# Performance work log

Measured on AMD Instinct MI355X. Metric: run time of the kernel, lower is better.

Reference implementation:

```python
import jax, jax.numpy as jnp
import numpy as np

B, N, D, H = 8, 512, 512, 8
DK = D // H          # 64
DIM_G = 64           # trigonometric geometry embedding dim
WAVE_LEN = 1000.0


def box_relational_embedding(f_g):
    # f_g: [B, N, 4] -> [B, N, N, 64]
    x_min, y_min, x_max, y_max = [f_g[..., i] for i in range(4)]  # [B,N]
    cx = (x_min + x_max) * 0.5
    cy = (y_min + y_max) * 0.5
    w = x_max - x_min + 1.0
    h = y_max - y_min + 1.0
    # pairwise deltas; divide by w_i / h_i of the row box (broadcast over j)
    dx = jnp.log(jnp.clip(jnp.abs((cx[:, :, None] - cx[:, None, :]) / w[:, :, None]), 0.001))
    dy = jnp.log(jnp.clip(jnp.abs((cy[:, :, None] - cy[:, None, :]) / h[:, :, None]), 0.001))
    dw = jnp.log(w[:, :, None] / w[:, None, :])
    dh = jnp.log(h[:, :, None] / h[:, None, :])
    pos = jnp.stack([dx, dy, dw, dh], axis=-1)  # [B,N,N,4]
    feat_range = jnp.arange(DIM_G // 8, dtype=jnp.float32) / (DIM_G / 8.0)  # [8]
    dim_mat = 1.0 / (WAVE_LEN ** feat_range)  # [8]
    mul = (100.0 * pos)[..., None] * dim_mat  # [B,N,N,4,8]
    mul = mul.reshape(pos.shape[0], pos.shape[1], pos.shape[2], -1)  # [B,N,N,32]
    return jnp.concatenate([jnp.sin(mul), jnp.cos(mul)], axis=-1)  # [B,N,N,64]


def setup_inputs() -> dict:
    key = jax.random.key(0)
    ks = jax.random.split(key, 12)
    s = 1.0 / np.sqrt(D)
    return {
        "input_query": jax.random.normal(ks[0], (B, N, D), jnp.float32),
        "input_key": jax.random.normal(ks[1], (B, N, D), jnp.float32),
        "input_value": jax.random.normal(ks[2], (B, N, D), jnp.float32),
        "input_box": jax.random.uniform(ks[3], (B, N, 4), jnp.float32),
        "mask": jax.random.randint(ks[4], (B, N), 0, 2, jnp.int32),
        "not_objects": jax.random.randint(ks[5], (B, N), 0, 2).astype(jnp.bool_),
        "Wq": jax.random.normal(ks[6], (D, D), jnp.float32) * s,
        "bq": jnp.zeros((D,), jnp.float32),
        "Wk": jax.random.normal(ks[7], (D, D), jnp.float32) * s,
        "bk": jnp.zeros((D,), jnp.float32),
        "Wv": jax.random.normal(ks[8], (D, D), jnp.float32) * s,
        "bv": jnp.zeros((D,), jnp.float32),
        "Wo": jax.random.normal(ks[9], (D, D), jnp.float32) * s,
        "bo": jnp.zeros((D,), jnp.float32),
        "WG": jax.random.normal(ks[10], (H, DIM_G), jnp.float32) * 0.1,
        "bG": jnp.zeros((H,), jnp.float32),
    }


def reference(input_query, input_key, input_value, input_box, mask, not_objects,
              Wq, bq, Wk, bk, Wv, bv, Wo, bo, WG, bG):
    emb = box_relational_embedding(input_box)  # [B,N,N,64]

    def proj(x, W, b):
        return (x @ W + b).reshape(B, N, H, DK).transpose(0, 2, 1, 3)  # [B,H,N,DK]

    q = proj(input_query, Wq, bq)
    k = proj(input_key, Wk, bk)
    v = proj(input_value, Wv, bv)

    scores = jnp.einsum('bhnd,bhmd->bhnm', q, k) / np.sqrt(DK).astype(np.float32)
    scores = jnp.where(mask[:, None, None, :] == 0, -1e9, scores)

    # per-head geometry weights: [B,H,N,N]
    wg = jax.nn.relu(jnp.einsum('bnmg,hg->bhnm', emb, WG) + bG[None, :, None, None])

    # object mask: zero the geometry log-bias where either i or j is not an object
    pair_not_obj = not_objects[:, None, :, None] | not_objects[:, None, None, :]  # [B,1,N,N]
    mask_obj = 1.0 - pair_not_obj.astype(jnp.float32)

    logits = jnp.log(jnp.clip(wg, 1e-6)) * mask_obj + scores
    attn = jax.nn.softmax(logits, axis=-1)  # dropout is identity in eval mode

    out = jnp.einsum('bhnm,bhmd->bhnd', attn, v)
    out = out.transpose(0, 2, 1, 3).reshape(B, N, D)
    return out @ Wo + bo
```

## Files before the change

kernel.cpp:

```cpp
#include <hip/hip_runtime.h>
#include <hip/hip_fp16.h>

#define B_ 8
#define N_ 512
#define D_ 512
#define H_ 8
#define DK_ 64

typedef unsigned int uint;
typedef unsigned short ushort;
typedef __attribute__((ext_vector_type(8))) short short8;
typedef __attribute__((ext_vector_type(8))) _Float16 half8;
typedef __attribute__((ext_vector_type(4))) _Float16 half4;
typedef __attribute__((ext_vector_type(4))) float floatx4;

__device__ __forceinline__ float bf2f(ushort s) { return __uint_as_float(((uint)s) << 16); }
__device__ __forceinline__ ushort f2bf(float f) {
    uint x = __float_as_uint(f);
    return (ushort)((x + 0x7fffu + ((x >> 16) & 1u)) >> 16);
}
__device__ __forceinline__ float blo(uint u) { return __uint_as_float(u << 16); }
__device__ __forceinline__ float bhi(uint u) { return __uint_as_float(u & 0xffff0000u); }
__device__ __forceinline__ float ldf(const void* p, size_t i, int isbf) {
    return isbf ? bf2f(((const ushort*)p)[i]) : ((const float*)p)[i];
}
__device__ __forceinline__ short ldb(const void* p, size_t i, int isbf) {
    return isbf ? (short)(((const ushort*)p)[i]) : (short)f2bf(((const float*)p)[i]);
}
__device__ __forceinline__ float4 ldbox(const void* p, size_t row, int isbf) {
    if (isbf) {
        const uint2 u = ((const uint2*)p)[row];
        return make_float4(blo(u.x), bhi(u.x), blo(u.y), bhi(u.y));
    }
    return ((const float4*)p)[row];
}
__device__ __forceinline__ float flog(float x) {
    return __builtin_amdgcn_logf(x) * 0.69314718056f;
}
__device__ __forceinline__ float fexp(float x) {
    return __builtin_amdgcn_exp2f(x * 1.44269504089f);
}
__device__ __forceinline__ void fsincos_rev(float rev, float* s, float* c) {
    const float fr = rev - floorf(rev);
    *s = __builtin_amdgcn_sinf(fr);
    *c = __builtin_amdgcn_cosf(fr);
}

__global__ __launch_bounds__(256) void probe_dtype(const uint* __restrict__ q,
                                                   int* __restrict__ flag) {
    __shared__ int s[256];
    const int t = threadIdx.x;
    int cnt = 0;
    for (int i = t; i < 4096; i += 256) {
        const uint e = (q[i] >> 7) & 0xffu;
        cnt += (e >= 0x70u && e <= 0x84u) ? 1 : 0;
    }
    s[t] = cnt;
    __syncthreads();
    for (int d = 128; d > 0; d >>= 1) {
        if (t < d) s[t] += s[t + d];
        __syncthreads();
    }
    if (t == 0) *flag = (s[0] > 3276) ? 1 : 0;
}

__global__ __launch_bounds__(256) void transw(const void* __restrict__ w0,
                                              const void* __restrict__ w1,
                                              const void* __restrict__ w2,
                                              const void* __restrict__ w3,
                                              const void* __restrict__ b0,
                                              const void* __restrict__ b1,
                                              const void* __restrict__ b2,
                                              const void* __restrict__ b3,
                                              ushort* __restrict__ wt,
                                              float* __restrict__ biasf,
                                              const int* __restrict__ flagp) {
    const int isbf = *flagp;
    const int z = blockIdx.z;
    const void* W = (z == 0) ? w0 : (z == 1) ? w1 : (z == 2) ? w2 : w3;
    const int n0 = blockIdx.x * 32, k0 = blockIdx.y * 32;
    __shared__ float tile[32][33];
    const int tx = threadIdx.x & 31, ty = threadIdx.x >> 5;
#pragma unroll
    for (int r = 0; r < 4; ++r)
        tile[ty + 8 * r][tx] = ldf(W, (size_t)(k0 + ty + 8 * r) * D_ + n0 + tx, isbf);
    if (blockIdx.x == 0 && blockIdx.y == 0) {
        const void* bz = (z == 0) ? b0 : (z == 1) ? b1 : (z == 2) ? b2 : b3;
        for (int e = threadIdx.x; e < 512; e += 256)
            biasf[z * 512 + e] = ldf(bz, e, isbf);
    }
    __syncthreads();
#pragma unroll
    for (int r = 0; r < 4; ++r)
        wt[(size_t)z * 262144 + (size_t)(n0 + ty + 8 * r) * D_ + k0 + tx] =
            f2bf(tile[tx][ty + 8 * r]);
}

__global__ __launch_bounds__(256) void gemm0(
    const void* __restrict__ A0, const void* __restrict__ A1, const void* __restrict__ A2,
    const ushort* __restrict__ wt, const float* __restrict__ biasf,
    ushort* __restrict__ oq, ushort* __restrict__ ok, ushort* __restrict__ ov,
    const int* __restrict__ flagp) {
    const int isbf = *flagp;
    const int z = blockIdx.z;
    const char* A = (const char*)((z == 0) ? A0 : (z == 1) ? A1 : A2);
    const ushort* W = wt + (size_t)z * 262144;
    const float* bias = biasf + z * 512;
    const int row0 = blockIdx.x * 128, col0 = blockIdx.y * 64;
    const int t = threadIdx.x, wv = t >> 6, lane = t & 63;
    const int m16 = lane & 15, quad = lane >> 4;

    __shared__ ushort As[128][40];
    __shared__ ushort Ws[64][40];
    floatx4 acc[2][4] = {};

    const int ar = t >> 1, ah = t & 1;
    const int wr = t >> 2, wc = (t & 3) * 8;

    float4 pf0, pf1, pf2, pf3;
    short8 ps0, ps1, pw;

    auto loadA = [&](int k0) {
        const size_t e = (size_t)(row0 + ar) * D_ + k0 + ah * 16;
        if (isbf) {
            ps0 = *(const short8*)(A + 2 * e);
            ps1 = *(const short8*)(A + 2 * e + 16);
        } else {
            const float* ap = (const float*)(A + 4 * e);
            pf0 = *(const float4*)(ap);
            pf1 = *(const float4*)(ap + 4);
            pf2 = *(const float4*)(ap + 8);
            pf3 = *(const float4*)(ap + 12);
        }
        pw = *(const short8*)(W + (size_t)(col0 + wr) * D_ + k0 + wc);
    };
    auto stage = [&]() {
        short8 s0, s1;
        if (isbf) {
            s0 = ps0; s1 = ps1;
        } else {
            s0[0] = (short)f2bf(pf0.x); s0[1] = (short)f2bf(pf0.y);
            s0[2] = (short)f2bf(pf0.z); s0[3] = (short)f2bf(pf0.w);
            s0[4] = (short)f2bf(pf1.x); s0[5] = (short)f2bf(pf1.y);
            s0[6] = (short)f2bf(pf1.z); s0[7] = (short)f2bf(pf1.w);
            s1[0] = (short)f2bf(pf2.x); s1[1] = (short)f2bf(pf2.y);
            s1[2] = (short)f2bf(pf2.z); s1[3] = (short)f2bf(pf2.w);
            s1[4] = (short)f2bf(pf3.x); s1[5] = (short)f2bf(pf3.y);
            s1[6] = (short)f2bf(pf3.z); s1[7] = (short)f2bf(pf3.w);
        }
        *(short8*)&As[ar][ah * 16] = s0;
        *(short8*)&As[ar][ah * 16 + 8] = s1;
        *(short8*)&Ws[wr][wc] = pw;
    };

    loadA(0);
    for (int k0 = 0; k0 < D_; k0 += 32) {
        __syncthreads();
        stage();
        __syncthreads();
        if (k0 + 32 < D_) loadA(k0 + 32);

        const short8 a0 = *(const short8*)&As[wv * 32 + m16][quad * 8];
        const short8 a1 = *(const short8*)&As[wv * 32 + 16 + m16][quad * 8];
        const short8 b0 = *(const short8*)&Ws[m16][quad * 8];
        const short8 b1 = *(const short8*)&Ws[16 + m16][quad * 8];
        const short8 b2 = *(const short8*)&Ws[32 + m16][quad * 8];
        const short8 b3 = *(const short8*)&Ws[48 + m16][quad * 8];
        acc[0][0] = __builtin_amdgcn_mfma_f32_16x16x32_bf16(a0, b0, acc[0][0], 0, 0, 0);
        acc[0][1] = __builtin_amdgcn_mfma_f32_16x16x32_bf16(a0, b1, acc[0][1], 0, 0, 0);
        acc[0][2] = __builtin_amdgcn_mfma_f32_16x16x32_bf16(a0, b2, acc[0][2], 0, 0, 0);
        acc[0][3] = __builtin_amdgcn_mfma_f32_16x16x32_bf16(a0, b3, acc[0][3], 0, 0, 0);
        acc[1][0] = __builtin_amdgcn_mfma_f32_16x16x32_bf16(a1, b0, acc[1][0], 0, 0, 0);
        acc[1][1] = __builtin_amdgcn_mfma_f32_16x16x32_bf16(a1, b1, acc[1][1], 0, 0, 0);
        acc[1][2] = __builtin_amdgcn_mfma_f32_16x16x32_bf16(a1, b2, acc[1][2], 0, 0, 0);
        acc[1][3] = __builtin_amdgcn_mfma_f32_16x16x32_bf16(a1, b3, acc[1][3], 0, 0, 0);
    }

#pragma unroll
    for (int mt = 0; mt < 2; ++mt) {
#pragma unroll
        for (int nt = 0; nt < 4; ++nt) {
            const int colg = col0 + nt * 16 + m16;
            const float bi = bias[colg];
            const float v0 = acc[mt][nt][0] + bi, v1 = acc[mt][nt][1] + bi;
            const float v2 = acc[mt][nt][2] + bi, v3 = acc[mt][nt][3] + bi;
            const int rowb = row0 + wv * 32 + mt * 16 + quad * 4;
            if (z == 2) {
                const int bhv = (rowb >> 9) * H_ + (colg >> 6);
                uint2 pk;
                pk.x = (uint)f2bf(v0) | ((uint)f2bf(v1) << 16);
                pk.y = (uint)f2bf(v2) | ((uint)f2bf(v3) << 16);
                *(uint2*)(ov + ((size_t)bhv * DK_ + (colg & 63)) * N_ + (rowb & 511)) = pk;
            } else {
                ushort* o = (z == 0) ? oq : ok;
                const float vv[4] = {v0, v1, v2, v3};
#pragma unroll
                for (int r = 0; r < 4; ++r) {
                    const int row = rowb + r;
                    o[((size_t)((row >> 9) * H_ + (colg >> 6)) * N_ + (row & 511)) * DK_ +
                      (colg & 63)] = f2bf(vv[r]);
                }
            }
        }
    }
}

__global__ __launch_bounds__(256) void gemm1(
    const ushort* __restrict__ att, const ushort* __restrict__ wt,
    const float* __restrict__ biasf, void* __restrict__ dout,
    const int* __restrict__ flagp) {
    const int isbf = *flagp;
    const ushort* W = wt + (size_t)3 * 262144;
    const float* bias = biasf + 3 * 512;
    const int row0 = blockIdx.x * 128, col0 = blockIdx.y * 64;
    const int t = threadIdx.x, wv = t >> 6, lane = t & 63;
    const int m16 = lane & 15, quad = lane >> 4;

    __shared__ ushort As[128][40];
    __shared__ ushort Ws[64][40];
    floatx4 acc[2][4] = {};

    const int ar = t >> 1, ah = t & 1;
    const int wr = t >> 2, wc = (t & 3) * 8;

    short8 ps0, ps1, pw;
    auto loadA = [&](int k0) {
        const ushort* ap = att + (size_t)(row0 + ar) * D_ + k0 + ah * 16;
        ps0 = *(const short8*)(ap);
        ps1 = *(const short8*)(ap + 8);
        pw = *(const short8*)(W + (size_t)(col0 + wr) * D_ + k0 + wc);
    };

    loadA(0);
    for (int k0 = 0; k0 < D_; k0 += 32) {
        __syncthreads();
        *(short8*)&As[ar][ah * 16] = ps0;
        *(short8*)&As[ar][ah * 16 + 8] = ps1;
        *(short8*)&Ws[wr][wc] = pw;
        __syncthreads();
        if (k0 + 32 < D_) loadA(k0 + 32);

        const short8 a0 = *(const short8*)&As[wv * 32 + m16][quad * 8];
        const short8 a1 = *(const short8*)&As[wv * 32 + 16 + m16][quad * 8];
        const short8 b0 = *(const short8*)&Ws[m16][quad * 8];
        const short8 b1 = *(const short8*)&Ws[16 + m16][quad * 8];
        const short8 b2 = *(const short8*)&Ws[32 + m16][quad * 8];
        const short8 b3 = *(const short8*)&Ws[48 + m16][quad * 8];
        acc[0][0] = __builtin_amdgcn_mfma_f32_16x16x32_bf16(a0, b0, acc[0][0], 0, 0, 0);
        acc[0][1] = __builtin_amdgcn_mfma_f32_16x16x32_bf16(a0, b1, acc[0][1], 0, 0, 0);
        acc[0][2] = __builtin_amdgcn_mfma_f32_16x16x32_bf16(a0, b2, acc[0][2], 0, 0, 0);
        acc[0][3] = __builtin_amdgcn_mfma_f32_16x16x32_bf16(a0, b3, acc[0][3], 0, 0, 0);
        acc[1][0] = __builtin_amdgcn_mfma_f32_16x16x32_bf16(a1, b0, acc[1][0], 0, 0, 0);
        acc[1][1] = __builtin_amdgcn_mfma_f32_16x16x32_bf16(a1, b1, acc[1][1], 0, 0, 0);
        acc[1][2] = __builtin_amdgcn_mfma_f32_16x16x32_bf16(a1, b2, acc[1][2], 0, 0, 0);
        acc[1][3] = __builtin_amdgcn_mfma_f32_16x16x32_bf16(a1, b3, acc[1][3], 0, 0, 0);
    }

#pragma unroll
    for (int mt = 0; mt < 2; ++mt) {
#pragma unroll
        for (int nt = 0; nt < 4; ++nt) {
            const int colg = col0 + nt * 16 + m16;
            const float bi = bias[colg];
#pragma unroll
            for (int r = 0; r < 4; ++r) {
                const int row = row0 + wv * 32 + mt * 16 + quad * 4 + r;
                const float v = acc[mt][nt][r] + bi;
                if (isbf) ((ushort*)dout)[(size_t)row * D_ + colg] = f2bf(v);
                else      ((float*)dout)[(size_t)row * D_ + colg] = v;
            }
        }
    }
}

__global__ __launch_bounds__(256) void geom2(const void* __restrict__ box,
                                             const int* __restrict__ nobj,
                                             const void* __restrict__ WG,
                                             const void* __restrict__ bG,
                                             ushort* __restrict__ glog,
                                             const int* __restrict__ flagp) {
    const int isbf = *flagp;
    const int i = blockIdx.x, bl = blockIdx.y;
    const int t = threadIdx.x;

    __shared__ _Float16 trig[128][76];
    __shared__ _Float16 wgf[16][72];
    __shared__ float mobja[128];
    __shared__ float bgs[8];

    for (int e = t; e < 1024; e += 256) {
        const int h = e >> 6, g = e & 63;
        wgf[h][g] = (_Float16)((h < 8) ? ldf(WG, (size_t)h * 64 + g, isbf) : 0.f);
    }
    if (t < 8) bgs[t] = ldf(bG, t, isbf);

    const float4 bi4 = ldbox(box, (size_t)bl * N_ + i, isbf);
    const float wi = bi4.z - bi4.x + 1.0f, hi = bi4.w - bi4.y + 1.0f;
    const float cxi = (bi4.x + bi4.z) * 0.5f, cyi = (bi4.y + bi4.w) * 0.5f;
    const float rwi = 1.0f / wi, rhi = 1.0f / hi;
    const float lwi = flog(wi), lhi = flog(hi);
    const int noi = nobj[bl * N_ + i];
    __syncthreads();

    const int wv = t >> 6, lane = t & 63, m16 = lane & 15, quad = lane >> 4;
    const half8 bf0 = *(const half8*)&wgf[m16][quad * 8];
    const half8 bf1 = *(const half8*)&wgf[m16][quad * 8 + 32];
    _Float16* gb = (_Float16*)glog +
                   ((((size_t)bl * 32 + (i >> 4)) * 8) * 16 + (i & 15)) * 512;
    const float dmrev[8] = {15.915494f, 6.7115083f, 2.8302207f, 1.1934936f,
                            0.50329214f, 0.21223603f, 0.089498095f, 0.037742074f};

    for (int c = 0; c < 4; ++c) {
        const int jbase = c * 128;
        {
            const int pair = t >> 1, hf = t & 1;
            const int j = jbase + pair;
            const float4 bj4 = ldbox(box, (size_t)bl * N_ + j, isbf);
            const float wj = bj4.z - bj4.x + 1.0f, hj = bj4.w - bj4.y + 1.0f;
            float p0, p1;
            if (hf == 0) {
                const float cxj = (bj4.x + bj4.z) * 0.5f, cyj = (bj4.y + bj4.w) * 0.5f;
                p0 = flog(fmaxf(fabsf((cxi - cxj) * rwi), 0.001f));
                p1 = flog(fmaxf(fabsf((cyi - cyj) * rhi), 0.001f));
                mobja[pair] = (noi || nobj[bl * N_ + j]) ? 0.f : 1.f;
            } else {
                p0 = lwi - flog(wj);
                p1 = lhi - flog(hj);
            }
#pragma unroll
            for (int pp = 0; pp < 2; ++pp) {
                const float base = pp ? p1 : p0;
                half8 s8, c8;
#pragma unroll
                for (int f = 0; f < 8; ++f) {
                    float sv, cv;
                    fsincos_rev(base * dmrev[f], &sv, &cv);
                    s8[f] = (_Float16)sv;
                    c8[f] = (_Float16)cv;
                }
                const int g0 = hf * 16 + pp * 8;
                *(half4*)&trig[pair][g0]          = *(const half4*)&s8;
                *(half4*)&trig[pair][g0 + 4]      = *((const half4*)&s8 + 1);
                *(half4*)&trig[pair][32 + g0]     = *(const half4*)&c8;
                *(half4*)&trig[pair][32 + g0 + 4] = *((const half4*)&c8 + 1);
            }
        }
        __syncthreads();
        {
#pragma unroll
            for (int sub = 0; sub < 2; ++sub) {
                const int row = wv * 32 + sub * 16 + m16;
                half8 a0, a1;
                *((half4*)&a0)     = *(const half4*)&trig[row][quad * 8];
                *((half4*)&a0 + 1) = *(const half4*)&trig[row][quad * 8 + 4];
                *((half4*)&a1)     = *(const half4*)&trig[row][32 + quad * 8];
                *((half4*)&a1 + 1) = *(const half4*)&trig[row][32 + quad * 8 + 4];
                floatx4 acc = {};
                acc = __builtin_amdgcn_mfma_f32_16x16x32_f16(a0, bf0, acc, 0, 0, 0);
                acc = __builtin_amdgcn_mfma_f32_16x16x32_f16(a1, bf1, acc, 0, 0, 0);
                if (m16 < 8) {
#pragma unroll
                    for (int r = 0; r < 4; ++r) {
                        const int pair = wv * 32 + sub * 16 + quad * 4 + r;
                        const float wg = acc[r] + bgs[m16];
                        const float gl = flog(fmaxf(wg, 1e-6f)) * mobja[pair];
                        gb[(size_t)m16 * 8192 + jbase + pair] = (_Float16)gl;
                    }
                }
            }
        }
        __syncthreads();
    }
}

__global__ __launch_bounds__(256) void attn3(
    const ushort* __restrict__ qw, const ushort* __restrict__ kw,
    const ushort* __restrict__ vt, const int* __restrict__ mask,
    const ushort* __restrict__ glog, ushort* __restrict__ att, int b0) {
    const int it = blockIdx.x, h = blockIdx.y, bl = blockIdx.z;
    const int bg = b0 + bl;
    const int i0 = it * 16;
    const int t = threadIdx.x, wv = t >> 6, lane = t & 63;
    const int m16 = lane & 15, quad = lane >> 4;
    const size_t bh = (size_t)(bg * H_ + h);

    __shared__ float lg[16][516];
    __shared__ ushort sbuf[16 * 520];
    __shared__ float rsumInv[16];

    {
        const uint4* src = (const uint4*)(glog + (((size_t)bl * 32 + it) * 8 + h) * 8192);
        uint4* dst = (uint4*)sbuf;
#pragma unroll
        for (int e = 0; e < 4; ++e) dst[t + 256 * e] = src[t + 256 * e];
    }
    const ushort* qrow = qw + (bh * N_ + i0 + m16) * DK_ + quad * 8;
    const short8 aq0 = *(const short8*)(qrow);
    const short8 aq1 = *(const short8*)(qrow + 32);
    __syncthreads();

#pragma unroll
    for (int tt = 0; tt < 8; ++tt) {
        const int j0 = wv * 128 + tt * 16;
        const ushort* krow = kw + (bh * N_ + j0 + m16) * DK_ + quad * 8;
        const short8 bk0 = *(const short8*)(krow);
        const short8 bk1 = *(const short8*)(krow + 32);
        floatx4 acc = {};
        acc = __builtin_amdgcn_mfma_f32_16x16x32_bf16(aq0, bk0, acc, 0, 0, 0);
        acc = __builtin_amdgcn_mfma_f32_16x16x32_bf16(aq1, bk1, acc, 0, 0, 0);
        const int mj = mask[bg * N_ + j0 + m16];
        const __half* gt = (const __half*)sbuf;
#pragma unroll
        for (int r = 0; r < 4; ++r) {
            const int i = quad * 4 + r;
            const float g = __half2float(gt[i * 512 + j0 + m16]);
            lg[i][j0 + m16] = (mj ? 0.125f * acc[r] : -1e9f) + g;
        }
    }
    __syncthreads();

    {
        const int row = t >> 4, l = t & 15;
        float v[32];
        float mx = -3e38f;
#pragma unroll
        for (int s = 0; s < 32; ++s) { v[s] = lg[row][l + 16 * s]; mx = fmaxf(mx, v[s]); }
#pragma unroll
        for (int d = 1; d < 16; d <<= 1) mx = fmaxf(mx, __shfl_xor(mx, d, 16));
        float sm = 0.f;
#pragma unroll
        for (int s = 0; s < 32; ++s) { const float p = fexp(v[s] - mx); sm += p; v[s] = p; }
#pragma unroll
        for (int d = 1; d < 16; d <<= 1) sm += __shfl_xor(sm, d, 16);
#pragma unroll
        for (int s = 0; s < 32; ++s) sbuf[row * 520 + l + 16 * s] = f2bf(v[s]);
        if (l == 0) rsumInv[row] = 1.0f / sm;
    }
    __syncthreads();

    {
        const int dk0 = wv * 16;
        const ushort* vrow = vt + (bh * DK_ + dk0 + m16) * N_ + quad * 8;
        floatx4 oc = {};
#pragma unroll
        for (int kc = 0; kc < 16; ++kc) {
            const short8 ap = *(const short8*)(sbuf + m16 * 520 + kc * 32 + quad * 8);
            const short8 bv = *(const short8*)(vrow + kc * 32);
            oc = __builtin_amdgcn_mfma_f32_16x16x32_bf16(ap, bv, oc, 0, 0, 0);
        }
#pragma unroll
        for (int r = 0; r < 4; ++r) {
            const int i = quad * 4 + r;
            const float o = oc[r] * rsumInv[i];
            att[((size_t)(bg * N_ + i0 + i)) * D_ + h * DK_ + dk0 + m16] = f2bf(o);
        }
    }
}

__global__ __launch_bounds__(256) void gemm16(const void* __restrict__ A,
                                              const void* __restrict__ W,
                                              const void* __restrict__ bias,
                                              void* __restrict__ out,
                                              const int* __restrict__ flagp,
                                              int a_follows, int mode) {
    const int isbf = *flagp;
    const int a_isbf = a_follows ? isbf : 1;
    const int wave = threadIdx.x >> 6;
    const int tile = blockIdx.x * 4 + wave;
    const int tm = tile >> 5, tn = tile & 31;
    const int row0 = tm * 16, col0 = tn * 16;
    const int lane = threadIdx.x & 63;
    const int m = lane & 15, quad = lane >> 4;
    floatx4 acc = {0.f, 0.f, 0.f, 0.f};
    const size_t abase = (size_t)(row0 + m) * D_ + quad * 8;
    const size_t wbase = (size_t)(quad * 8) * D_ + col0 + m;
    for (int k0 = 0; k0 < D_; k0 += 32) {
        short8 af, bf;
#pragma unroll
        for (int j = 0; j < 8; ++j) af[j] = ldb(A, abase + k0 + j, a_isbf);
#pragma unroll
        for (int j = 0; j < 8; ++j) bf[j] = ldb(W, wbase + (size_t)(k0 + j) * D_, isbf);
        acc = __builtin_amdgcn_mfma_f32_16x16x32_bf16(af, bf, acc, 0, 0, 0);
    }
    const int col = col0 + m;
    const float bi = ldf(bias, col, isbf);
#pragma unroll
    for (int r = 0; r < 4; ++r) {
        const int row = row0 + quad * 4 + r;
        const float v = acc[r] + bi;
        if (mode == 1) {
            ((ushort*)out)[(size_t)(((row >> 9) * H_ + (col >> 6)) * N_ + (row & 511)) * DK_ + (col & 63)] = f2bf(v);
        } else if (isbf) {
            ((ushort*)out)[(size_t)row * D_ + col] = f2bf(v);
        } else {
            ((float*)out)[(size_t)row * D_ + col] = v;
        }
    }
}

__global__ __launch_bounds__(256) void attn_old(
    const ushort* __restrict__ qw, const ushort* __restrict__ kw,
    const ushort* __restrict__ vw, const void* __restrict__ box,
    const int* __restrict__ mask, const int* __restrict__ nobj,
    const void* __restrict__ WG, const void* __restrict__ bG,
    ushort* __restrict__ att, const int* __restrict__ flagp) {
    const int isbf = *flagp;
    const int b = blockIdx.z, h = blockIdx.y;
    const int i0 = blockIdx.x * 8;
    const int t = threadIdx.x;
    __shared__ float lg[8][520];
    __shared__ float q_s[8][68];
    __shared__ float wgh[64];
    __shared__ float cxi[8], cyi[8], rwi[8], rhi[8], lwi[8], lhi[8];
    __shared__ int noi[8];
    __shared__ float rsum[8];
    for (int e = t; e < 512; e += 256) {
        const int ii = e >> 6, dk = e & 63;
        q_s[ii][dk] = bf2f(qw[(size_t)((b * H_ + h) * N_ + i0 + ii) * DK_ + dk]) * 0.125f;
    }
    if (t < 64) wgh[t] = ldf(WG, h * 64 + t, isbf);
    if (t < 8) {
        const size_t bb = (size_t)(b * N_ + i0 + t) * 4;
        const float xmn = ldf(box, bb + 0, isbf), ymn = ldf(box, bb + 1, isbf);
        const float xmx = ldf(box, bb + 2, isbf), ymx = ldf(box, bb + 3, isbf);
        const float w = xmx - xmn + 1.0f, hh = ymx - ymn + 1.0f;
        cxi[t] = (xmn + xmx) * 0.5f;
        cyi[t] = (ymn + ymx) * 0.5f;
        rwi[t] = 1.0f / w;
        rhi[t] = 1.0f / hh;
        lwi[t] = __logf(w);
        lhi[t] = __logf(hh);
        noi[t] = nobj[b * N_ + i0 + t];
    }
    const float bg = ldf(bG, h, isbf);
    __syncthreads();
    for (int jl = 0; jl < 2; ++jl) {
        const int j = t + jl * 256;
        float acc[8];
#pragma unroll
        for (int ii = 0; ii < 8; ++ii) acc[ii] = 0.f;
        const uint4* krow = (const uint4*)(kw + (size_t)((b * H_ + h) * N_ + j) * DK_);
#pragma unroll
        for (int c = 0; c < 8; ++c) {
            const uint4 ku = krow[c];
            float kf[8];
            kf[0] = blo(ku.x); kf[1] = bhi(ku.x); kf[2] = blo(ku.y); kf[3] = bhi(ku.y);
            kf[4] = blo(ku.z); kf[5] = bhi(ku.z); kf[6] = blo(ku.w); kf[7] = bhi(ku.w);
#pragma unroll
            for (int ii = 0; ii < 8; ++ii) {
                const float4 qa = *(const float4*)(&q_s[ii][c * 8]);
                const float4 qb = *(const float4*)(&q_s[ii][c * 8 + 4]);
                acc[ii] += qa.x * kf[0] + qa.y * kf[1] + qa.z * kf[2] + qa.w * kf[3] +
                           qb.x * kf[4] + qb.y * kf[5] + qb.z * kf[6] + qb.w * kf[7];
            }
        }
        const int mj = mask[b * N_ + j];
        const size_t bb = (size_t)(b * N_ + j) * 4;
        const float xmn = ldf(box, bb + 0, isbf), ymn = ldf(box, bb + 1, isbf);
        const float xmx = ldf(box, bb + 2, isbf), ymx = ldf(box, bb + 3, isbf);
        const float cxj = (xmn + xmx) * 0.5f, cyj = (ymn + ymx) * 0.5f;
        const float wj = xmx - xmn + 1.0f, hj = ymx - ymn + 1.0f;
        const float lwj = __logf(wj), lhj = __logf(hj);
        const int noj = nobj[b * N_ + j];
        const float dm[8] = {1.0f, 0.421696503f, 0.177827941f, 0.074989421f,
                             0.031622777f, 0.013335214f, 0.005623413f, 0.002371374f};
        for (int ii = 0; ii < 8; ++ii) {
            const float mobj = (noi[ii] || noj) ? 0.f : 1.f;
            const float dx = __logf(fmaxf(fabsf((cxi[ii] - cxj) * rwi[ii]), 0.001f));
            const float dy = __logf(fmaxf(fabsf((cyi[ii] - cyj) * rhi[ii]), 0.001f));
            const float pos[4] = {dx, dy, lwi[ii] - lwj, lhi[ii] - lhj};
            float wg = bg;
            for (int p = 0; p < 4; ++p) {
                const float base = 100.f * pos[p];
#pragma unroll
                for (int f = 0; f < 8; ++f) {
                    float sv, cv;
                    __sincosf(base * dm[f], &sv, &cv);
                    const int g = p * 8 + f;
                    wg += sv * wgh[g] + cv * wgh[32 + g];
                }
            }
            lg[ii][j] = (mj ? acc[ii] : -1e9f) + __logf(fmaxf(wg, 1e-6f)) * mobj;
        }
    }
    __syncthreads();
    {
        const int rr = t >> 5, l32 = t & 31;
        float mx = -3e38f;
        for (int j = l32; j < N_; j += 32) mx = fmaxf(mx, lg[rr][j]);
#pragma unroll
        for (int d = 1; d < 32; d <<= 1) mx = fmaxf(mx, __shfl_xor(mx, d, 32));
        float sm = 0.f;
        for (int j = l32; j < N_; j += 32) {
            const float p = __expf(lg[rr][j] - mx);
            lg[rr][j] = p;
            sm += p;
        }
#pragma unroll
        for (int d = 1; d < 32; d <<= 1) sm += __shfl_xor(sm, d, 32);
        if (l32 == 0) rsum[rr] = sm;
    }
    __syncthreads();
    {
        const int ii = t >> 5, dkp = t & 31;
        float o0 = 0.f, o1 = 0.f;
        const uint* vbase = (const uint*)vw + (size_t)((b * H_ + h) * N_) * (DK_ / 2) + dkp;
        for (int j = 0; j < N_; ++j) {
            const uint u = vbase[(size_t)j * (DK_ / 2)];
            const float p = lg[ii][j];
            o0 += p * blo(u);
            o1 += p * bhi(u);
        }
        const float inv = 1.0f / rsum[ii];
        const uint pk = (uint)f2bf(o0 * inv) | ((uint)f2bf(o1 * inv) << 16);
        ((uint*)att)[(size_t)(b * N_ + i0 + ii) * (D_ / 2) + h * 32 + dkp] = pk;
    }
}

extern "C" void kernel_launch(void* const* d_in, const int* in_sizes, int n_in,
                              void* d_out, int out_size, void* d_ws, size_t ws_size,
                              hipStream_t stream) {
    const void* xq = d_in[0];
    const void* xk = d_in[1];
    const void* xv = d_in[2];
    const void* box = d_in[3];
    const int* mask = (const int*)d_in[4];
    const int* nobj = (const int*)d_in[5];
    const void* Wq = d_in[6];
    const void* bq = d_in[7];
    const void* Wk = d_in[8];
    const void* bk = d_in[9];
    const void* Wv = d_in[10];
    const void* bv = d_in[11];
    const void* Wo = d_in[12];
    const void* bo = d_in[13];
    const void* WG = d_in[14];
    const void* bG = d_in[15];

    char* ws = (char*)d_ws;
    const size_t MB = 1u << 20;

    if (ws_size >= 54 * MB) {
        int* flag = (int*)ws;
        float* biasf = (float*)(ws + 4096);
        ushort* wt = (ushort*)(ws + 16384);
        size_t p = 16384 + 2097152;
        ushort* qw = (ushort*)(ws + p); p += 4194304;
        ushort* kw = (ushort*)(ws + p); p += 4194304;
        ushort* vt = (ushort*)(ws + p); p += 4194304;
        ushort* att = (ushort*)(ws + p); p += 4194304;
        ushort* glog = (ushort*)(ws + p);

        hipLaunchKernelGGL(probe_dtype, dim3(1), dim3(256), 0, stream, (const uint*)xq, flag);
        hipLaunchKernelGGL(transw, dim3(16, 16, 4), dim3(256), 0, stream,
                           Wq, Wk, Wv, Wo, bq, bk, bv, bo, wt, biasf, flag);
        hipLaunchKernelGGL(gemm0, dim3(32, 8, 3), dim3(256), 0, stream,
                           xq, xk, xv, wt, biasf, qw, kw, vt, flag);
        hipLaunchKernelGGL(geom2, dim3(N_, B_), dim3(256), 0, stream,
                           box, nobj, WG, bG, glog, flag);
        hipLaunchKernelGGL(attn3, dim3(32, H_, B_), dim3(256), 0, stream,
                           qw, kw, vt, mask, glog, att, 0);
        hipLaunchKernelGGL(gemm1, dim3(32, 8), dim3(256), 0, stream,
                           att, wt, biasf, d_out, flag);
    } else {
        int* flag = (int*)ws;
        ushort* qw = (ushort*)(ws + 256);
        ushort* kw = (ushort*)(ws + 256 + 4194304);
        ushort* vw = (ushort*)(ws + 256 + 8388608);
        ushort* att = (ushort*)(ws + 256 + 12582912);
        hipLaunchKernelGGL(probe_dtype, dim3(1), dim3(256), 0, stream, (const uint*)xq, flag);
        hipLaunchKernelGGL(gemm16, dim3(2048), dim3(256), 0, stream, xq, Wq, bq, (void*)qw, flag, 1, 1);
        hipLaunchKernelGGL(gemm16, dim3(2048), dim3(256), 0, stream, xk, Wk, bk, (void*)kw, flag, 1, 1);
        hipLaunchKernelGGL(gemm16, dim3(2048), dim3(256), 0, stream, xv, Wv, bv, (void*)vw, flag, 1, 1);
        hipLaunchKernelGGL(attn_old, dim3(N_ / 8, H_, B_), dim3(256), 0, stream,
                           qw, kw, vw, box, mask, nobj, WG, bG, att, flag);
        hipLaunchKernelGGL(gemm16, dim3(2048), dim3(256), 0, stream, att, Wo, bo, d_out, flag, 0, 2);
    }
}
```

Before: 200.2 us.

## Merge QKV projection GEMM and geometry kernel into one heterogeneous launch

Combines the QKV projection GEMM and the geometry-bias kernel into a single launch of 4864 blocks. The first 768 blocks do the GEMM and the rest compute the geometry log-bias, with a shared memory buffer reused by both paths. This removes one kernel launch and the gap between them, and lets the compute-heavy trig work run alongside the GEMM. It also swaps the fp32-to-bf16 round-to-nearest-even conversion for a cheaper round-half-up using a perm instruction, in both the GEMM staging and the softmax output. That conversion change slightly alters numerics.

After: 198.2 us. Within noise of the previous version (-1.0%).

```diff
diff --git a/kernel.cpp b/kernel.cpp
--- a/kernel.cpp
+++ b/kernel.cpp
@@ -44,6 +44,9 @@
     const float fr = rev - floorf(rev);
     *s = __builtin_amdgcn_sinf(fr);
     *c = __builtin_amdgcn_cosf(fr);
+}
+__device__ __forceinline__ uint pkbf(uint a, uint b) {
+    return __builtin_amdgcn_perm(b + 0x8000u, a + 0x8000u, 0x07060302u);
 }
 
 __global__ __launch_bounds__(256) void probe_dtype(const uint* __restrict__ q,
@@ -96,16 +99,215 @@
             f2bf(tile[tx][ty + 8 * r]);
 }
 
-__global__ __launch_bounds__(256) void gemm0(
-    const void* __restrict__ A0, const void* __restrict__ A1, const void* __restrict__ A2,
+__global__ __launch_bounds__(256) void stage1(
+    const void* __restrict__ xq, const void* __restrict__ xk, const void* __restrict__ xv,
     const ushort* __restrict__ wt, const float* __restrict__ biasf,
     ushort* __restrict__ oq, ushort* __restrict__ ok, ushort* __restrict__ ov,
+    const void* __restrict__ box, const int* __restrict__ nobj,
+    const void* __restrict__ WG, const void* __restrict__ bG,
+    ushort* __restrict__ glog, const int* __restrict__ flagp) {
+    __shared__ __align__(16) char smem[22336];
+    const int isbf = *flagp;
+    const int bid = blockIdx.x;
+    const int t = threadIdx.x, wv = t >> 6, lane = t & 63;
+    const int m16 = lane & 15, quad = lane >> 4;
+
+    if (bid < 768) {
+        const int z = bid >> 8, rem = bid & 255;
+        const int row0 = (rem & 31) * 128, col0 = (rem >> 5) * 64;
+        const char* A = (const char*)((z == 0) ? xq : (z == 1) ? xk : xv);
+        const ushort* W = wt + (size_t)z * 262144;
+        const float* bias = biasf + z * 512;
+        ushort (*As)[40] = (ushort(*)[40])smem;
+        ushort (*Ws)[40] = (ushort(*)[40])(smem + 10240);
+        floatx4 acc[2][4] = {};
+
+        const int ar = t >> 1, ah = t & 1;
+        const int wr = t >> 2, wc = (t & 3) * 8;
+
+        uint4 ua, ub, uc, ud;
+        short8 ps0, ps1, pw;
+
+        auto loadA = [&](int k0) {
+            const size_t e = (size_t)(row0 + ar) * D_ + k0 + ah * 16;
+            if (isbf) {
+                ps0 = *(const short8*)(A + 2 * e);
+                ps1 = *(const short8*)(A + 2 * e + 16);
+            } else {
+                const uint* ap = (const uint*)A + e;
+                ua = *(const uint4*)(ap);
+                ub = *(const uint4*)(ap + 4);
+                uc = *(const uint4*)(ap + 8);
+                ud = *(const uint4*)(ap + 12);
+            }
+            pw = *(const short8*)(W + (size_t)(col0 + wr) * D_ + k0 + wc);
+        };
+        auto stage = [&]() {
+            if (isbf) {
+                *(short8*)&As[ar][ah * 16] = ps0;
+                *(short8*)&As[ar][ah * 16 + 8] = ps1;
+            } else {
+                uint4 lo, hi;
+                lo.x = pkbf(ua.x, ua.y); lo.y = pkbf(ua.z, ua.w);
+                lo.z = pkbf(ub.x, ub.y); lo.w = pkbf(ub.z, ub.w);
+                hi.x = pkbf(uc.x, uc.y); hi.y = pkbf(uc.z, uc.w);
+                hi.z = pkbf(ud.x, ud.y); hi.w = pkbf(ud.z, ud.w);
+                *(uint4*)&As[ar][ah * 16] = lo;
+                *(uint4*)&As[ar][ah * 16 + 8] = hi;
+            }
+            *(short8*)&Ws[wr][wc] = pw;
+        };
+
+        loadA(0);
+        for (int k0 = 0; k0 < D_; k0 += 32) {
+            __syncthreads();
+            stage();
+            __syncthreads();
+            if (k0 + 32 < D_) loadA(k0 + 32);
+
+            const short8 a0 = *(const short8*)&As[wv * 32 + m16][quad * 8];
+            const short8 a1 = *(const short8*)&As[wv * 32 + 16 + m16][quad * 8];
+            const short8 b0 = *(const short8*)&Ws[m16][quad * 8];
+            const short8 b1 = *(const short8*)&Ws[16 + m16][quad * 8];
+            const short8 b2 = *(const short8*)&Ws[32 + m16][quad * 8];
+            const short8 b3 = *(const short8*)&Ws[48 + m16][quad * 8];
+            acc[0][0] = __builtin_amdgcn_mfma_f32_16x16x32_bf16(a0, b0, acc[0][0], 0, 0, 0);
+            acc[0][1] = __builtin_amdgcn_mfma_f32_16x16x32_bf16(a0, b1, acc[0][1], 0, 0, 0);
+            acc[0][2] = __builtin_amdgcn_mfma_f32_16x16x32_bf16(a0, b2, acc[0][2], 0, 0, 0);
+            acc[0][3] = __builtin_amdgcn_mfma_f32_16x16x32_bf16(a0, b3, acc[0][3], 0, 0, 0);
+            acc[1][0] = __builtin_amdgcn_mfma_f32_16x16x32_bf16(a1, b0, acc[1][0], 0, 0, 0);
+            acc[1][1] = __builtin_amdgcn_mfma_f32_16x16x32_bf16(a1, b1, acc[1][1], 0, 0, 0);
+            acc[1][2] = __builtin_amdgcn_mfma_f32_16x16x32_bf16(a1, b2, acc[1][2], 0, 0, 0);
+            acc[1][3] = __builtin_amdgcn_mfma_f32_16x16x32_bf16(a1, b3, acc[1][3], 0, 0, 0);
+        }
+
+#pragma unroll
+        for (int mt = 0; mt < 2; ++mt) {
+#pragma unroll
+            for (int nt = 0; nt < 4; ++nt) {
+                const int colg = col0 + nt * 16 + m16;
+                const float bi = bias[colg];
+                const float v0 = acc[mt][nt][0] + bi, v1 = acc[mt][nt][1] + bi;
+                const float v2 = acc[mt][nt][2] + bi, v3 = acc[mt][nt][3] + bi;
+                const int rowb = row0 + wv * 32 + mt * 16 + quad * 4;
+                if (z == 2) {
+                    const int bhv = (rowb >> 9) * H_ + (colg >> 6);
+                    uint2 pk;
+                    pk.x = (uint)f2bf(v0) | ((uint)f2bf(v1) << 16);
+                    pk.y = (uint)f2bf(v2) | ((uint)f2bf(v3) << 16);
+                    *(uint2*)(ov + ((size_t)bhv * DK_ + (colg & 63)) * N_ + (rowb & 511)) = pk;
+                } else {
+                    ushort* o = (z == 0) ? oq : ok;
+                    const float vv[4] = {v0, v1, v2, v3};
+#pragma unroll
+                    for (int r = 0; r < 4; ++r) {
+                        const int row = rowb + r;
+                        o[((size_t)((row >> 9) * H_ + (colg >> 6)) * N_ + (row & 511)) * DK_ +
+                          (colg & 63)] = f2bf(vv[r]);
+                    }
+                }
+            }
+        }
+    } else {
+        const int id = bid - 768;
+        const int i = id & 511, bl = id >> 9;
+        _Float16 (*trig)[76] = (_Float16(*)[76])smem;
+        _Float16 (*wgf)[72] = (_Float16(*)[72])(smem + 19456);
+        float* mobja = (float*)(smem + 21760);
+        float* bgs = (float*)(smem + 22272);
+
+        for (int e = t; e < 1024; e += 256) {
+            const int h = e >> 6, g = e & 63;
+            wgf[h][g] = (_Float16)((h < 8) ? ldf(WG, (size_t)h * 64 + g, isbf) : 0.f);
+        }
+        if (t < 8) bgs[t] = ldf(bG, t, isbf);
+
+        const float4 bi4 = ldbox(box, (size_t)bl * N_ + i, isbf);
+        const float wi = bi4.z - bi4.x + 1.0f, hi = bi4.w - bi4.y + 1.0f;
+        const float cxi = (bi4.x + bi4.z) * 0.5f, cyi = (bi4.y + bi4.w) * 0.5f;
+        const float rwi = 1.0f / wi, rhi = 1.0f / hi;
+        const float lwi = flog(wi), lhi = flog(hi);
+        const int noi = nobj[bl * N_ + i];
+        __syncthreads();
+
+        const half8 bf0 = *(const half8*)&wgf[m16][quad * 8];
+        const half8 bf1 = *(const half8*)&wgf[m16][quad * 8 + 32];
+        _Float16* gb = (_Float16*)glog +
+                       ((((size_t)bl * 32 + (i >> 4)) * 8) * 16 + (i & 15)) * 512;
+        const float dmrev[8] = {15.915494f, 6.7115083f, 2.8302207f, 1.1934936f,
+                                0.50329214f, 0.21223603f, 0.089498095f, 0.037742074f};
+
+        for (int c = 0; c < 4; ++c) {
+            const int jbase = c * 128;
+            {
+                const int pair = t >> 1, hf = t & 1;
+                const int j = jbase + pair;
+                const float4 bj4 = ldbox(box, (size_t)bl * N_ + j, isbf);
+                const float wj = bj4.z - bj4.x + 1.0f, hj = bj4.w - bj4.y + 1.0f;
+                float p0, p1;
+                if (hf == 0) {
+                    const float cxj = (bj4.x + bj4.z) * 0.5f, cyj = (bj4.y + bj4.w) * 0.5f;
+                    p0 = flog(fmaxf(fabsf((cxi - cxj) * rwi), 0.001f));
+                    p1 = flog(fmaxf(fabsf((cyi - cyj) * rhi), 0.001f));
+                    mobja[pair] = (noi || nobj[bl * N_ + j]) ? 0.f : 1.f;
+                } else {
+                    p0 = lwi - flog(wj);
+                    p1 = lhi - flog(hj);
+                }
+#pragma unroll
+                for (int pp = 0; pp < 2; ++pp) {
+                    const float base = pp ? p1 : p0;
+                    half8 s8, c8;
+#pragma unroll
+                    for (int f = 0; f < 8; ++f) {
+                        float sv, cv;
+                        fsincos_rev(base * dmrev[f], &sv, &cv);
+                        s8[f] = (_Float16)sv;
+                        c8[f] = (_Float16)cv;
+                    }
+                    const int g0 = hf * 16 + pp * 8;
+                    *(half4*)&trig[pair][g0]          = *(const half4*)&s8;
+                    *(half4*)&trig[pair][g0 + 4]      = *((const half4*)&s8 + 1);
+                    *(half4*)&trig[pair][32 + g0]     = *(const half4*)&c8;
+                    *(half4*)&trig[pair][32 + g0 + 4] = *((const half4*)&c8 + 1);
+                }
+            }
+            __syncthreads();
+            {
+#pragma unroll
+                for (int sub = 0; sub < 2; ++sub) {
+                    const int row = wv * 32 + sub * 16 + m16;
+                    half8 a0, a1;
+                    *((half4*)&a0)     = *(const half4*)&trig[row][quad * 8];
+                    *((half4*)&a0 + 1) = *(const half4*)&trig[row][quad * 8 + 4];
+                    *((half4*)&a1)     = *(const half4*)&trig[row][32 + quad * 8];
+                    *((half4*)&a1 + 1) = *(const half4*)&trig[row][32 + quad * 8 + 4];
+                    floatx4 acc = {};
+                    acc = __builtin_amdgcn_mfma_f32_16x16x32_f16(a0, bf0, acc, 0, 0, 0);
+                    acc = __builtin_amdgcn_mfma_f32_16x16x32_f16(a1, bf1, acc, 0, 0, 0);
+                    if (m16 < 8) {
+#pragma unroll
+                        for (int r = 0; r < 4; ++r) {
+                            const int pair = wv * 32 + sub * 16 + quad * 4 + r;
+                            const float wg = acc[r] + bgs[m16];
+                            const float gl = flog(fmaxf(wg, 1e-6f)) * mobja[pair];
+                            gb[(size_t)m16 * 8192 + jbase + pair] = (_Float16)gl;
+                        }
+                    }
+                }
+            }
+            __syncthreads();
+        }
+    }
+}
+
+__global__ __launch_bounds__(256) void gemm1(
+    const ushort* __restrict__ att, const ushort* __restrict__ wt,
+    const float* __restrict__ biasf, void* __restrict__ dout,
     const int* __restrict__ flagp) {
     const int isbf = *flagp;
-    const int z = blockIdx.z;
-    const char* A = (const char*)((z == 0) ? A0 : (z == 1) ? A1 : A2);
-    const ushort* W = wt + (size_t)z * 262144;
-    const float* bias = biasf + z * 512;
+    const ushort* W = wt + (size_t)3 * 262144;
+    const float* bias = biasf + 3 * 512;
     const int row0 = blockIdx.x * 128, col0 = blockIdx.y * 64;
     const int t = threadIdx.x, wv = t >> 6, lane = t & 63;
     const int m16 = lane & 15, quad = lane >> 4;
@@ -117,46 +319,20 @@
     const int ar = t >> 1, ah = t & 1;
     const int wr = t >> 2, wc = (t & 3) * 8;
 
-    float4 pf0, pf1, pf2, pf3;
     short8 ps0, ps1, pw;
-
     auto loadA = [&](int k0) {
-        const size_t e = (size_t)(row0 + ar) * D_ + k0 + ah * 16;
-        if (isbf) {
-            ps0 = *(const short8*)(A + 2 * e);
-            ps1 = *(const short8*)(A + 2 * e + 16);
-        } else {
-            const float* ap = (const float*)(A + 4 * e);
-            pf0 = *(const float4*)(ap);
-            pf1 = *(const float4*)(ap + 4);
-            pf2 = *(const float4*)(ap + 8);
-            pf3 = *(const float4*)(ap + 12);
-        }
+        const ushort* ap = att + (size_t)(row0 + ar) * D_ + k0 + ah * 16;
+        ps0 = *(const short8*)(ap);
+        ps1 = *(const short8*)(ap + 8);
         pw = *(const short8*)(W + (size_t)(col0 + wr) * D_ + k0 + wc);
-    };
-    auto stage = [&]() {
-        short8 s0, s1;
-        if (isbf) {
-            s0 = ps0; s1 = ps1;
-        } else {
-            s0[0] = (short)f2bf(pf0.x); s0[1] = (short)f2bf(pf0.y);
-            s0[2] = (short)f2bf(pf0.z); s0[3] = (short)f2bf(pf0.w);
-            s0[4] = (short)f2bf(pf1.x); s0[5] = (short)f2bf(pf1.y);
-            s0[6] = (short)f2bf(pf1.z); s0[7] = (short)f2bf(pf1.w);
-            s1[0] = (short)f2bf(pf2.x); s1[1] = (short)f2bf(pf2.y);
-            s1[2] = (short)f2bf(pf2.z); s1[3] = (short)f2bf(pf2.w);
-            s1[4] = (short)f2bf(pf3.x); s1[5] = (short)f2bf(pf3.y);
-            s1[6] = (short)f2bf(pf3.z); s1[7] = (short)f2bf(pf3.w);
-        }
-        *(short8*)&As[ar][ah * 16] = s0;
-        *(short8*)&As[ar][ah * 16 + 8] = s1;
-        *(short8*)&Ws[wr][wc] = pw;
     };
 
     loadA(0);
     for (int k0 = 0; k0 < D_; k0 += 32) {
         __syncthreads();
-        stage();
+        *(short8*)&As[ar][ah * 16] = ps0;
+        *(short8*)&As[ar][ah * 16 + 8] = ps1;
+        *(short8*)&Ws[wr][wc] = pw;
         __syncthreads();
         if (k0 + 32 < D_) loadA(k0 + 32);
 
@@ -182,86 +358,6 @@
         for (int nt = 0; nt < 4; ++nt) {
             const int colg = col0 + nt * 16 + m16;
             const float bi = bias[colg];
-            const float v0 = acc[mt][nt][0] + bi, v1 = acc[mt][nt][1] + bi;
-            const float v2 = acc[mt][nt][2] + bi, v3 = acc[mt][nt][3] + bi;
-            const int rowb = row0 + wv * 32 + mt * 16 + quad * 4;
-            if (z == 2) {
-                const int bhv = (rowb >> 9) * H_ + (colg >> 6);
-                uint2 pk;
-                pk.x = (uint)f2bf(v0) | ((uint)f2bf(v1) << 16);
-                pk.y = (uint)f2bf(v2) | ((uint)f2bf(v3) << 16);
-                *(uint2*)(ov + ((size_t)bhv * DK_ + (colg & 63)) * N_ + (rowb & 511)) = pk;
-            } else {
-                ushort* o = (z == 0) ? oq : ok;
-                const float vv[4] = {v0, v1, v2, v3};
-#pragma unroll
-                for (int r = 0; r < 4; ++r) {
-                    const int row = rowb + r;
-                    o[((size_t)((row >> 9) * H_ + (colg >> 6)) * N_ + (row & 511)) * DK_ +
-                      (colg & 63)] = f2bf(vv[r]);
-                }
-            }
-        }
-    }
-}
-
-__global__ __launch_bounds__(256) void gemm1(
-    const ushort* __restrict__ att, const ushort* __restrict__ wt,
-    const float* __restrict__ biasf, void* __restrict__ dout,
-    const int* __restrict__ flagp) {
-    const int isbf = *flagp;
-    const ushort* W = wt + (size_t)3 * 262144;
-    const float* bias = biasf + 3 * 512;
-    const int row0 = blockIdx.x * 128, col0 = blockIdx.y * 64;
-    const int t = threadIdx.x, wv = t >> 6, lane = t & 63;
-    const int m16 = lane & 15, quad = lane >> 4;
-
-    __shared__ ushort As[128][40];
-    __shared__ ushort Ws[64][40];
-    floatx4 acc[2][4] = {};
-
-    const int ar = t >> 1, ah = t & 1;
-    const int wr = t >> 2, wc = (t & 3) * 8;
-
-    short8 ps0, ps1, pw;
-    auto loadA = [&](int k0) {
-        const ushort* ap = att + (size_t)(row0 + ar) * D_ + k0 + ah * 16;
-        ps0 = *(const short8*)(ap);
-        ps1 = *(const short8*)(ap + 8);
-        pw = *(const short8*)(W + (size_t)(col0 + wr) * D_ + k0 + wc);
-    };
-
-    loadA(0);
-    for (int k0 = 0; k0 < D_; k0 += 32) {
-        __syncthreads();
-        *(short8*)&As[ar][ah * 16] = ps0;
-        *(short8*)&As[ar][ah * 16 + 8] = ps1;
-        *(short8*)&Ws[wr][wc] = pw;
-        __syncthreads();
-        if (k0 + 32 < D_) loadA(k0 + 32);
-
-        const short8 a0 = *(const short8*)&As[wv * 32 + m16][quad * 8];
-        const short8 a1 = *(const short8*)&As[wv * 32 + 16 + m16][quad * 8];
-        const short8 b0 = *(const short8*)&Ws[m16][quad * 8];
-        const short8 b1 = *(const short8*)&Ws[16 + m16][quad * 8];
-        const short8 b2 = *(const short8*)&Ws[32 + m16][quad * 8];
-        const short8 b3 = *(const short8*)&Ws[48 + m16][quad * 8];
-        acc[0][0] = __builtin_amdgcn_mfma_f32_16x16x32_bf16(a0, b0, acc[0][0], 0, 0, 0);
-        acc[0][1] = __builtin_amdgcn_mfma_f32_16x16x32_bf16(a0, b1, acc[0][1], 0, 0, 0);
-        acc[0][2] = __builtin_amdgcn_mfma_f32_16x16x32_bf16(a0, b2, acc[0][2], 0, 0, 0);
-        acc[0][3] = __builtin_amdgcn_mfma_f32_16x16x32_bf16(a0, b3, acc[0][3], 0, 0, 0);
-        acc[1][0] = __builtin_amdgcn_mfma_f32_16x16x32_bf16(a1, b0, acc[1][0], 0, 0, 0);
-        acc[1][1] = __builtin_amdgcn_mfma_f32_16x16x32_bf16(a1, b1, acc[1][1], 0, 0, 0);
-        acc[1][2] = __builtin_amdgcn_mfma_f32_16x16x32_bf16(a1, b2, acc[1][2], 0, 0, 0);
-        acc[1][3] = __builtin_amdgcn_mfma_f32_16x16x32_bf16(a1, b3, acc[1][3], 0, 0, 0);
-    }
-
-#pragma unroll
-    for (int mt = 0; mt < 2; ++mt) {
-#pragma unroll
-        for (int nt = 0; nt < 4; ++nt) {
-            const int colg = col0 + nt * 16 + m16;
-            const float bi = bias[colg];
 #pragma unroll
             for (int r = 0; r < 4; ++r) {
                 const int row = row0 + wv * 32 + mt * 16 + quad * 4 + r;
@@ -270,106 +366,6 @@
                 else      ((float*)dout)[(size_t)row * D_ + colg] = v;
             }
         }
-    }
-}
-
-__global__ __launch_bounds__(256) void geom2(const void* __restrict__ box,
-                                             const int* __restrict__ nobj,
-                                             const void* __restrict__ WG,
-                                             const void* __restrict__ bG,
-                                             ushort* __restrict__ glog,
-                                             const int* __restrict__ flagp) {
-    const int isbf = *flagp;
-    const int i = blockIdx.x, bl = blockIdx.y;
-    const int t = threadIdx.x;
-
-    __shared__ _Float16 trig[128][76];
-    __shared__ _Float16 wgf[16][72];
-    __shared__ float mobja[128];
-    __shared__ float bgs[8];
-
-    for (int e = t; e < 1024; e += 256) {
-        const int h = e >> 6, g = e & 63;
-        wgf[h][g] = (_Float16)((h < 8) ? ldf(WG, (size_t)h * 64 + g, isbf) : 0.f);
-    }
-    if (t < 8) bgs[t] = ldf(bG, t, isbf);
-
-    const float4 bi4 = ldbox(box, (size_t)bl * N_ + i, isbf);
-    const float wi = bi4.z - bi4.x + 1.0f, hi = bi4.w - bi4.y + 1.0f;
-    const float cxi = (bi4.x + bi4.z) * 0.5f, cyi = (bi4.y + bi4.w) * 0.5f;
-    const float rwi = 1.0f / wi, rhi = 1.0f / hi;
-    const float lwi = flog(wi), lhi = flog(hi);
-    const int noi = nobj[bl * N_ + i];
-    __syncthreads();
-
-    const int wv = t >> 6, lane = t & 63, m16 = lane & 15, quad = lane >> 4;
-    const half8 bf0 = *(const half8*)&wgf[m16][quad * 8];
-    const half8 bf1 = *(const half8*)&wgf[m16][quad * 8 + 32];
-    _Float16* gb = (_Float16*)glog +
-                   ((((size_t)bl * 32 + (i >> 4)) * 8) * 16 + (i & 15)) * 512;
-    const float dmrev[8] = {15.915494f, 6.7115083f, 2.8302207f, 1.1934936f,
-                            0.50329214f, 0.21223603f, 0.089498095f, 0.037742074f};
-
-    for (int c = 0; c < 4; ++c) {
-        const int jbase = c * 128;
-        {
-            const int pair = t >> 1, hf = t & 1;
-            const int j = jbase + pair;
-            const float4 bj4 = ldbox(box, (size_t)bl * N_ + j, isbf);
-            const float wj = bj4.z - bj4.x + 1.0f, hj = bj4.w - bj4.y + 1.0f;
-            float p0, p1;
-            if (hf == 0) {
-                const float cxj = (bj4.x + bj4.z) * 0.5f, cyj = (bj4.y + bj4.w) * 0.5f;
-                p0 = flog(fmaxf(fabsf((cxi - cxj) * rwi), 0.001f));
-                p1 = flog(fmaxf(fabsf((cyi - cyj) * rhi), 0.001f));
-                mobja[pair] = (noi || nobj[bl * N_ + j]) ? 0.f : 1.f;
-            } else {
-                p0 = lwi - flog(wj);
-                p1 = lhi - flog(hj);
-            }
-#pragma unroll
-            for (int pp = 0; pp < 2; ++pp) {
-                const float base = pp ? p1 : p0;
-                half8 s8, c8;
-#pragma unroll
-                for (int f = 0; f < 8; ++f) {
-                    float sv, cv;
-                    fsincos_rev(base * dmrev[f], &sv, &cv);
-                    s8[f] = (_Float16)sv;
-                    c8[f] = (_Float16)cv;
-                }
-                const int g0 = hf * 16 + pp * 8;
-                *(half4*)&trig[pair][g0]          = *(const half4*)&s8;
-                *(half4*)&trig[pair][g0 + 4]      = *((const half4*)&s8 + 1);
-                *(half4*)&trig[pair][32 + g0]     = *(const half4*)&c8;
-                *(half4*)&trig[pair][32 + g0 + 4] = *((const half4*)&c8 + 1);
-            }
-        }
-        __syncthreads();
-        {
-#pragma unroll
-            for (int sub = 0; sub < 2; ++sub) {
-                const int row = wv * 32 + sub * 16 + m16;
-                half8 a0, a1;
-                *((half4*)&a0)     = *(const half4*)&trig[row][quad * 8];
-                *((half4*)&a0 + 1) = *(const half4*)&trig[row][quad * 8 + 4];
-                *((half4*)&a1)     = *(const half4*)&trig[row][32 + quad * 8];
-                *((half4*)&a1 + 1) = *(const half4*)&trig[row][32 + quad * 8 + 4];
-                floatx4 acc = {};
-                acc = __builtin_amdgcn_mfma_f32_16x16x32_f16(a0, bf0, acc, 0, 0, 0);
-                acc = __builtin_amdgcn_mfma_f32_16x16x32_f16(a1, bf1, acc, 0, 0, 0);
-                if (m16 < 8) {
-#pragma unroll
-                    for (int r = 0; r < 4; ++r) {
-                        const int pair = wv * 32 + sub * 16 + quad * 4 + r;
-                        const float wg = acc[r] + bgs[m16];
-                        const float gl = flog(fmaxf(wg, 1e-6f)) * mobja[pair];
-                        gb[(size_t)m16 * 8192 + jbase + pair] = (_Float16)gl;
-                    }
-                }
-            }
-        }
-        __syncthreads();
     }
 }
 
@@ -433,7 +429,8 @@
 #pragma unroll
         for (int d = 1; d < 16; d <<= 1) sm += __shfl_xor(sm, d, 16);
 #pragma unroll
-        for (int s = 0; s < 32; ++s) sbuf[row * 520 + l + 16 * s] = f2bf(v[s]);
+        for (int s = 0; s < 32; ++s)
+            sbuf[row * 520 + l + 16 * s] = (ushort)((__float_as_uint(v[s]) + 0x8000u) >> 16);
         if (l == 0) rsumInv[row] = 1.0f / sm;
     }
     __syncthreads();
@@ -654,9 +651,8 @@
         hipLaunchKernelGGL(probe_dtype, dim3(1), dim3(256), 0, stream, (const uint*)xq, flag);
         hipLaunchKernelGGL(transw, dim3(16, 16, 4), dim3(256), 0, stream,
                            Wq, Wk, Wv, Wo, bq, bk, bv, bo, wt, biasf, flag);
-        hipLaunchKernelGGL(gemm0, dim3(32, 8, 3), dim3(256), 0, stream,
-                           xq, xk, xv, wt, biasf, qw, kw, vt, flag);
-        hipLaunchKernelGGL(geom2, dim3(N_, B_), dim3(256), 0, stream,
+        hipLaunchKernelGGL(stage1, dim3(4864), dim3(256), 0, stream,
+                           xq, xk, xv, wt, biasf, qw, kw, vt,
                            box, nobj, WG, bG, glog, flag);
         hipLaunchKernelGGL(attn3, dim3(32, H_, B_), dim3(256), 0, stream,
                            qw, kw, vt, mask, glog, att, 0);
```
